# Optimization experiments

Hardware: AMD Instinct MI355X
Metric: run time of the kernel (lower is better)

The kernel has to match this reference:

```python
import jax, jax.numpy as jnp
import numpy as np

B, C, H, W = 4, 256, 64, 64
SCALE, K, COMP, G = 2, 5, 4, 1
MID = max(C // COMP, 16)                 # 64
ENC_OUT = K * K * SCALE * SCALE * G      # 100


def setup_inputs() -> dict:
    key = jax.random.key(0)
    k1, k2, k3 = jax.random.split(key, 3)
    x = jax.random.normal(k1, (B, C, H, W), jnp.float32)
    # comp: 1x1 conv C -> MID (store as matrix), enc: 3x3 conv MID -> ENC_OUT
    W_comp = jax.random.normal(k2, (MID, C), jnp.float32) * (1.0 / np.sqrt(C))
    b_comp = jnp.zeros((MID,), jnp.float32)
    W_enc = jax.random.normal(k3, (ENC_OUT, MID, 3, 3), jnp.float32) * (1.0 / np.sqrt(MID * 9))
    b_enc = jnp.zeros((ENC_OUT,), jnp.float32)
    return {"x": x, "W_comp": W_comp, "b_comp": b_comp, "W_enc": W_enc, "b_enc": b_enc}


def _unfold(x, k):
    """torch F.unfold with padding=(k-1)//2 -> (b, c, k*k, h, w), kh-major then kw."""
    b, c, h, w = x.shape
    p = (k - 1) // 2
    xp = jnp.pad(x, ((0, 0), (0, 0), (p, p), (p, p)))
    patches = jnp.stack(
        [xp[:, :, i:i + h, j:j + w] for i in range(k) for j in range(k)], axis=2
    )
    return patches  # (b, c, k*k, h, w)


def _carafe(x, W_comp, b_comp, W_enc, b_enc):
    b, c, h, w = x.shape
    s, k, g = SCALE, K, G
    # 1x1 compress conv + inplace relu
    feat = jax.nn.relu(jnp.einsum('bchw,mc->bmhw', x, W_comp) + b_comp[None, :, None, None])
    # 3x3 kernel-encoder conv, padding=1 (SAME)
    wk = jax.lax.conv_general_dilated(
        feat, W_enc, window_strides=(1, 1), padding='SAME',
        dimension_numbers=('NCHW', 'OIHW', 'NCHW')
    ) + b_enc[None, :, None, None]
    wk = wk.reshape(b, g, s * s, k * k, h, w)
    wk = jax.nn.softmax(wk, axis=3)  # softmax over k*k taps
    # unfold input and do the content-aware weighted gather-sum without the
    # (b,g,c/g,s*s,k*k,h,w) blow-up: contract over the k*k tap axis directly.
    xu = _unfold(x, k).reshape(b, g, c // g, k * k, h, w)
    out = jnp.einsum('bgpkhw,bgckhw->bgcphw', wk, xu)  # (b,g,c/g,s*s,h,w)
    # pixel rearrangement exactly as in the torch code:
    # view(b,c,s*s,h,w) -> permute(0,1,3,4,2) -> view(b,c,h*s,w*s)
    out = out.reshape(b, c, s * s, h, w)
    out = jnp.transpose(out, (0, 1, 3, 4, 2))
    out = out.reshape(b, c, h * s, w * s)
    return out


def reference(x, W_comp, b_comp, W_enc, b_enc):
    return _carafe(x, W_comp, b_comp, W_enc, b_enc)
```

## Files before the change

kernel.cpp:

```cpp
#include <hip/hip_runtime.h>

#define OFF_FEAT 0
#define OFF_WET  1048576
#define OFF_WCT  1122304
#define OFF_WK   1138688
#define WS_FLOATS 2777088

__global__ __launch_bounds__(256) void prep_kernel(
    const float* __restrict__ Wc, const float* __restrict__ We,
    float* __restrict__ ws) {
    int i = blockIdx.x * 256 + threadIdx.x;
    if (i < 16384) {
        int c = i >> 6, m = i & 63;
        ws[OFF_WCT + i] = Wc[m * 256 + c];
    }
    if (i < 73728) {
        int mrs = i >> 7, rem = i & 127;
        int p = rem >> 5, kk = rem & 31;
        ws[OFF_WET + i] = (kk < 25) ? We[(p * 25 + kk) * 576 + mrs] : 0.f;
    }
}

__global__ __launch_bounds__(256) void compress_kernel(
    const float* __restrict__ x, const float* __restrict__ bc,
    const float* __restrict__ ws, float* __restrict__ feat) {
    __shared__ float xs[64 * 64];
    int blk = blockIdx.x;
    int pxg = blk >> 2, mq = blk & 3;
    int pixbase = pxg * 64;
    int b = pixbase >> 12, pl = pixbase & 4095;
    int lane = threadIdx.x & 63;
    int chunk = __builtin_amdgcn_readfirstlane(threadIdx.x >> 6);
    int m0 = mq * 16 + chunk * 4;
    const float* wct = ws + OFF_WCT;
    float acc[4];
#pragma unroll
    for (int q = 0; q < 4; q++) acc[q] = 0.f;
    for (int h = 0; h < 4; h++) {
        int ch0 = h << 6;
        for (int idx = threadIdx.x; idx < 64 * 64; idx += 256) {
            int c = idx >> 6, pp = idx & 63;
            xs[idx] = x[((b * 256 + ch0 + c) << 12) + pl + pp];
        }
        __syncthreads();
        for (int c = 0; c < 64; c++) {
            float xv = xs[(c << 6) + lane];
            const float* wr = wct + (ch0 + c) * 64 + m0;
#pragma unroll
            for (int q = 0; q < 4; q++) acc[q] += xv * wr[q];
        }
        __syncthreads();
    }
#pragma unroll
    for (int q = 0; q < 4; q++) {
        int m = m0 + q;
        float v = acc[q] + bc[m];
        feat[(b * 64 + m) * 4096 + pl + lane] = v > 0.f ? v : 0.f;
    }
}

__global__ __launch_bounds__(512, 4) void enc_kernel(
    const float* __restrict__ be, const float* __restrict__ ws,
    float* __restrict__ wkout) {
    __shared__ float fs[4224];
    int t = threadIdx.x;
    int blk = blockIdx.x;
    int tile = blk >> 1, ph2 = blk & 1;
    int b = tile >> 6, t6 = tile & 63;
    int i0 = (t6 >> 3) << 3, j0 = (t6 & 7) << 3;
    int pix = t & 63;
    int li = pix >> 3, lj = pix & 7;
    int g = __builtin_amdgcn_readfirstlane(t >> 6);
    int pp = g >> 2;
    int p = (ph2 << 1) | pp;
    int k0 = (g & 3) << 3;
    const float* feat = ws + OFF_FEAT;
    const float* wet = ws + OFF_WET + p * 32 + k0;

    float acc[8];
#pragma unroll
    for (int q = 0; q < 8; q++) acc[q] = 0.f;

    for (int phase = 0; phase < 2; phase++) {
        int mb = phase << 5;
        for (int idx = t; idx < 3200; idx += 512) {
            int m = idx / 100, pos = idx - m * 100;
            int r = pos / 10, s = pos - r * 10;
            int gi = i0 + r - 1, gj = j0 + s - 1;
            float v = 0.f;
            if ((unsigned)gi < 64u && (unsigned)gj < 64u)
                v = feat[(b * 64 + mb + m) * 4096 + (gi << 6) + gj];
            fs[m * 120 + r * 12 + s] = v;
        }
        __syncthreads();

#pragma unroll 2
        for (int m = 0; m < 32; m++) {
            const float* fb = fs + m * 120 + li * 12 + lj;
            float f9[9];
#pragma unroll
            for (int r = 0; r < 3; r++)
#pragma unroll
                for (int s = 0; s < 3; s++) f9[r * 3 + s] = fb[r * 12 + s];
            const float* wrow = wet + (mb + m) * 1152;
#pragma unroll
            for (int rs = 0; rs < 9; rs++) {
                float f = f9[rs];
                const float* wr = wrow + rs * 128;
#pragma unroll
                for (int q = 0; q < 8; q++) acc[q] += f * wr[q];
            }
        }
        __syncthreads();
    }

#pragma unroll
    for (int q = 0; q < 8; q++) {
        int k = k0 + q;
        if (k < 25) fs[pix * 66 + pp * 33 + k] = acc[q] + be[p * 25 + k];
    }
    __syncthreads();

    if (t < 128) {
        int sp = t >> 6, spx = t & 63;
        const float* lg = fs + spx * 66 + sp * 33;
        float sv[25], mx = -1e30f;
#pragma unroll
        for (int k = 0; k < 25; k++) { sv[k] = lg[k]; mx = fmaxf(mx, sv[k]); }
        float s = 0.f;
#pragma unroll
        for (int k = 0; k < 25; k++) { sv[k] = __expf(sv[k] - mx); s += sv[k]; }
        float inv = 1.f / s;
        int preal = (ph2 << 1) | sp;
        int pgl = ((i0 + (spx >> 3)) << 6) + j0 + (spx & 7);
        float* wp = wkout + (preal * 25) * 16384 + (b << 12) + pgl;
#pragma unroll
        for (int k = 0; k < 25; k++) wp[k * 16384] = sv[k] * inv;
    }
}

__global__ __launch_bounds__(256) void gather_kernel(
    const float* __restrict__ x, const float* __restrict__ ws,
    float* __restrict__ out) {
    __shared__ float xs[16 * 5 * 68];
    int t = threadIdx.x;
    int blk = blockIdx.x;
    int cc = blk & 15;
    int bi = blk >> 4;
    int b = bi >> 6, i = bi & 63;
    int j = t & 63;
    int g = t >> 6;
    int ph = g >> 1, ch = g & 1;

    float w0[25], w1[25];
    {
        const float* wp = ws + OFF_WK + (ph * 50) * 16384 + (b << 12) + (i << 6) + j;
#pragma unroll
        for (int k = 0; k < 25; k++) {
            w0[k] = wp[k * 16384];
            w1[k] = wp[(25 + k) * 16384];
        }
    }

    {
        int lane = t & 63, cd0 = t >> 6;
        for (int cd = cd0; cd < 80; cd += 4) {
            int c = cd / 5, dy = cd - c * 5;
            int gi = i - 2 + dy;
            float v = 0.f;
            if ((unsigned)gi < 64u)
                v = x[((b * 256 + (cc << 4) + c) << 12) + (gi << 6) + lane];
            float* row = xs + cd * 68;
            row[2 + lane] = v;
            if (lane < 2) row[lane] = 0.f;
            if (lane >= 62) row[lane + 4] = 0.f;
        }
    }
    __syncthreads();

    for (int c2 = ch; c2 < 16; c2 += 2) {
        const float* xb = xs + (c2 * 5) * 68 + j;
        float a0 = 0.f, a1 = 0.f;
#pragma unroll
        for (int dy = 0; dy < 5; dy++) {
#pragma unroll
            for (int dx = 0; dx < 5; dx++) {
                float xv = xb[dy * 68 + dx];
                int k = dy * 5 + dx;
                a0 += xv * w0[k];
                a1 += xv * w1[k];
            }
        }
        int c = (cc << 4) + c2;
        float2 o2 = make_float2(a0, a1);
        *(float2*)(out + (((b * 256 + c) << 12) + (i << 6) + j) * 4 + ph * 2) = o2;
    }
}

__global__ __launch_bounds__(512) void carafe_fused(
    const float* __restrict__ x, const float* __restrict__ Wc,
    const float* __restrict__ bc, const float* __restrict__ We,
    const float* __restrict__ be, float* __restrict__ out) {
    __shared__ float xs[32 * 144];
    __shared__ float fw[6656];
    __shared__ float wst[3600];
    const int t = threadIdx.x;
    const int blk = blockIdx.x;
    const int b = blk >> 6, tile = blk & 63;
    const int i0 = (tile >> 3) << 3, j0 = (tile & 7) << 3;
    const int wid = t >> 6, pix = t & 63;
    const int li = pix >> 3, lj = pix & 7;
    float facc[13];
#pragma unroll
    for (int q = 0; q < 13; q++) facc[q] = 0.f;
    for (int cc = 0; cc < 8; cc++) {
        for (int idx = t; idx < 32 * 144; idx += 512) {
            int c = idx / 144, pos = idx - c * 144;
            int r = pos / 12, u = pos - r * 12;
            int gi = i0 + r - 2, gj = j0 + u - 2;
            float v = 0.f;
            if ((unsigned)gi < 64u && (unsigned)gj < 64u)
                v = x[(((b * 256 + cc * 32 + c) << 12) + (gi << 6) + gj)];
            xs[idx] = v;
        }
        __syncthreads();
#pragma unroll
        for (int q = 0; q < 13; q++) {
            int idx = q * 512 + t;
            if (idx < 6400) {
                int m = idx / 100, pos = idx - m * 100;
                int fi = pos / 10, fj = pos - fi * 10;
                int tp = (fi + 1) * 12 + fj + 1;
                const float* wr = Wc + m * 256 + cc * 32;
                float a = facc[q];
                for (int c = 0; c < 32; c++) a += xs[c * 144 + tp] * wr[c];
                facc[q] = a;
            }
        }
        __syncthreads();
    }
#pragma unroll
    for (int q = 0; q < 13; q++) {
        int idx = q * 512 + t;
        if (idx < 6400) {
            int m = idx / 100, pos = idx - m * 100;
            int fi = pos / 10, fj = pos - fi * 10;
            int gi = i0 + fi - 1, gj = j0 + fj - 1;
            float v = facc[q] + bc[m];
            v = v > 0.f ? v : 0.f;
            if ((unsigned)gi >= 64u || (unsigned)gj >= 64u) v = 0.f;
            fw[idx] = v;
        }
    }
    float acc[13];
#pragma unroll
    for (int q = 0; q < 13; q++) acc[q] = 0.f;
    for (int mb = 0; mb < 16; mb++) {
        for (int idx = t; idx < 3600; idx += 512) {
            int mm = idx / 900, rem = idx - mm * 900;
            int o = rem / 9, rs = rem - o * 9;
            wst[idx] = We[o * 576 + (mb * 4 + mm) * 9 + rs];
        }
        __syncthreads();
#pragma unroll
        for (int mm = 0; mm < 4; mm++) {
            const float* fb = fw + (mb * 4 + mm) * 100 + li * 10 + lj;
            float f9[9];
#pragma unroll
            for (int r = 0; r < 3; r++)
#pragma unroll
                for (int s = 0; s < 3; s++) f9[r * 3 + s] = fb[r * 10 + s];
#pragma unroll
            for (int q = 0; q < 13; q++) {
                int o = q * 8 + wid;
                if (o < 100) {
                    const float* wr = wst + mm * 900 + o * 9;
                    float a = acc[q];
#pragma unroll
                    for (int rs = 0; rs < 9; rs++) a += f9[rs] * wr[rs];
                    acc[q] = a;
                }
            }
        }
        __syncthreads();
    }
#pragma unroll
    for (int q = 0; q < 13; q++) {
        int o = q * 8 + wid;
        if (o < 100) fw[pix * 104 + o] = acc[q];
    }
    __syncthreads();
    float sv[25];
    float inv = 0.f;
    const int sp = t >> 6, spx = t & 63;
    const bool act = (t < 256);
    if (act) {
        float mx = -1e30f;
#pragma unroll
        for (int k = 0; k < 25; k++) {
            sv[k] = fw[spx * 104 + sp * 25 + k] + be[sp * 25 + k];
            mx = fmaxf(mx, sv[k]);
        }
        float s = 0.f;
#pragma unroll
        for (int k = 0; k < 25; k++) { sv[k] = __expf(sv[k] - mx); s += sv[k]; }
        inv = 1.f / s;
    }
    __syncthreads();
    if (act) {
#pragma unroll
        for (int k = 0; k < 25; k++) fw[spx * 104 + k * 4 + sp] = sv[k] * inv;
    }
    __syncthreads();
    float w[25][4];
    const float4* wp = (const float4*)(fw + pix * 104);
#pragma unroll
    for (int k = 0; k < 25; k++) {
        float4 ww = wp[k];
        w[k][0] = ww.x; w[k][1] = ww.y; w[k][2] = ww.z; w[k][3] = ww.w;
    }
    const int pgl = ((i0 + li) << 6) + (j0 + lj);
    for (int cc = 0; cc < 8; cc++) {
        for (int idx = t; idx < 32 * 144; idx += 512) {
            int c = idx / 144, pos = idx - c * 144;
            int r = pos / 12, u = pos - r * 12;
            int gi = i0 + r - 2, gj = j0 + u - 2;
            float v = 0.f;
            if ((unsigned)gi < 64u && (unsigned)gj < 64u)
                v = x[(((b * 256 + cc * 32 + c) << 12) + (gi << 6) + gj)];
            xs[idx] = v;
        }
        __syncthreads();
        for (int c8 = wid; c8 < 32; c8 += 8) {
            const float* xc = xs + c8 * 144 + li * 12 + lj;
            float a0 = 0.f, a1 = 0.f, a2 = 0.f, a3 = 0.f;
#pragma unroll
            for (int dy = 0; dy < 5; dy++) {
#pragma unroll
                for (int dx = 0; dx < 5; dx++) {
                    float xv = xc[dy * 12 + dx];
                    const int k = dy * 5 + dx;
                    a0 += xv * w[k][0];
                    a1 += xv * w[k][1];
                    a2 += xv * w[k][2];
                    a3 += xv * w[k][3];
                }
            }
            int c = cc * 32 + c8;
            float4 o4 = make_float4(a0, a1, a2, a3);
            *(float4*)(out + (((long long)(b * 256 + c)) << 14) + pgl * 4) = o4;
        }
        __syncthreads();
    }
}

extern "C" void kernel_launch(void* const* d_in, const int* in_sizes, int n_in,
                              void* d_out, int out_size, void* d_ws, size_t ws_size,
                              hipStream_t stream) {
    const float* x  = (const float*)d_in[0];
    const float* Wc = (const float*)d_in[1];
    const float* bc = (const float*)d_in[2];
    const float* We = (const float*)d_in[3];
    const float* be = (const float*)d_in[4];
    float* out = (float*)d_out;

    if (ws_size >= (size_t)WS_FLOATS * sizeof(float)) {
        float* ws = (float*)d_ws;
        prep_kernel<<<288, 256, 0, stream>>>(Wc, We, ws);
        compress_kernel<<<1024, 256, 0, stream>>>(x, bc, ws, ws + OFF_FEAT);
        enc_kernel<<<512, 512, 0, stream>>>(be, ws, ws + OFF_WK);
        gather_kernel<<<4096, 256, 0, stream>>>(x, ws, out);
    } else {
        carafe_fused<<<256, 512, 0, stream>>>(x, Wc, bc, We, be, out);
    }
}
```

Before: 188.6 us.

## Restructure compress conv to per-thread pixel with 32 output-channel register tile

```diff
diff --git a/kernel.cpp b/kernel.cpp
--- a/kernel.cpp
+++ b/kernel.cpp
@@ -24,38 +24,28 @@
 __global__ __launch_bounds__(256) void compress_kernel(
     const float* __restrict__ x, const float* __restrict__ bc,
     const float* __restrict__ ws, float* __restrict__ feat) {
-    __shared__ float xs[64 * 64];
     int blk = blockIdx.x;
-    int pxg = blk >> 2, mq = blk & 3;
-    int pixbase = pxg * 64;
+    int pxg = blk >> 1, mh = blk & 1;
+    int pixbase = pxg << 8;
     int b = pixbase >> 12, pl = pixbase & 4095;
-    int lane = threadIdx.x & 63;
-    int chunk = __builtin_amdgcn_readfirstlane(threadIdx.x >> 6);
-    int m0 = mq * 16 + chunk * 4;
-    const float* wct = ws + OFF_WCT;
-    float acc[4];
-#pragma unroll
-    for (int q = 0; q < 4; q++) acc[q] = 0.f;
-    for (int h = 0; h < 4; h++) {
-        int ch0 = h << 6;
-        for (int idx = threadIdx.x; idx < 64 * 64; idx += 256) {
-            int c = idx >> 6, pp = idx & 63;
-            xs[idx] = x[((b * 256 + ch0 + c) << 12) + pl + pp];
-        }
-        __syncthreads();
-        for (int c = 0; c < 64; c++) {
-            float xv = xs[(c << 6) + lane];
-            const float* wr = wct + (ch0 + c) * 64 + m0;
-#pragma unroll
-            for (int q = 0; q < 4; q++) acc[q] += xv * wr[q];
-        }
-        __syncthreads();
-    }
-#pragma unroll
-    for (int q = 0; q < 4; q++) {
-        int m = m0 + q;
-        float v = acc[q] + bc[m];
-        feat[(b * 64 + m) * 4096 + pl + lane] = v > 0.f ? v : 0.f;
+    int t = threadIdx.x;
+    const float* wct = ws + OFF_WCT + mh * 32;
+    const float* xp = x + (((long long)b * 256) << 12) + pl + t;
+    float acc[32];
+#pragma unroll
+    for (int q = 0; q < 32; q++) acc[q] = 0.f;
+#pragma unroll 4
+    for (int c = 0; c < 256; c++) {
+        float xv = xp[(size_t)c << 12];
+        const float* wr = wct + (c << 6);
+#pragma unroll
+        for (int q = 0; q < 32; q++) acc[q] += xv * wr[q];
+    }
+    int m0 = mh << 5;
+#pragma unroll
+    for (int q = 0; q < 32; q++) {
+        float v = acc[q] + bc[m0 + q];
+        feat[((b * 64 + m0 + q) << 12) + pl + t] = v > 0.f ? v : 0.f;
     }
 }
 
@@ -367,7 +357,7 @@
     if (ws_size >= (size_t)WS_FLOATS * sizeof(float)) {
         float* ws = (float*)d_ws;
         prep_kernel<<<288, 256, 0, stream>>>(Wc, We, ws);
-        compress_kernel<<<1024, 256, 0, stream>>>(x, bc, ws, ws + OFF_FEAT);
+        compress_kernel<<<128, 256, 0, stream>>>(x, bc, ws, ws + OFF_FEAT);
         enc_kernel<<<512, 512, 0, stream>>>(be, ws, ws + OFF_WK);
         gather_kernel<<<4096, 256, 0, stream>>>(x, ws, out);
     } else {
```

New measurement: 220.8 us. +17.1%, slower.
